# Kernel optimization log

Hardware: AMD Instinct MI355X
Metric: run time of the kernel (lower is better)

Reference implementation:

```python
import jax, jax.numpy as jnp
from jax import lax
import numpy as np

BLOCK_SIZE = 11   # cv2 blockSize (odd)
CONSTANT = 2.0    # cv2 C
MAXVAL = 255.0


def _box_mean(x, k):
    """Local k x k mean with BORDER_REPLICATE, matching cv2 ADAPTIVE_THRESH_MEAN_C.
    x: [N,H,W,1] float32. Separable 1-D box filters for efficiency."""
    pad = k // 2
    xp = jnp.pad(x, ((0, 0), (pad, pad), (pad, pad), (0, 0)), mode='edge')
    kh = jnp.full((k, 1, 1, 1), 1.0 / k, dtype=x.dtype)  # HWIO
    kw = jnp.full((1, k, 1, 1), 1.0 / k, dtype=x.dtype)
    dn = ('NHWC', 'HWIO', 'NHWC')
    y = lax.conv_general_dilated(xp, kh, (1, 1), 'VALID', dimension_numbers=dn)
    y = lax.conv_general_dilated(y, kw, (1, 1), 'VALID', dimension_numbers=dn)
    return y  # [N,H,W,1]


def setup_inputs() -> dict:
    key = jax.random.key(0)
    # grayscale pixel intensities in [0, 255]
    x = jax.random.uniform(key, (128, 512, 512, 1), dtype=jnp.float32) * 255.0
    return {"x": x}


def reference(x):
    # cv2.adaptiveThreshold(..., ADAPTIVE_THRESH_MEAN_C, THRESH_BINARY_INV, blockSize, C):
    #   T(x,y) = mean_{kxk}(src) - C
    #   dst = 0 if src > T else maxValue
    thresh = _box_mean(x, BLOCK_SIZE) - CONSTANT
    out = jnp.where(x > thresh, jnp.float32(0.0), jnp.float32(MAXVAL))
    return out
```

## Files before the change

### kernel.cpp

```cpp
#include <hip/hip_runtime.h>


constexpr int W   = 512;
constexpr int H   = 512;
constexpr int PAD = 5;
constexpr int KS  = 11;
constexpr int TPB = 256;
constexpr int RPB = 32;
constexpr int WP  = W + 2 * PAD;

__global__ __launch_bounds__(TPB)
void AdaptiveThresholding_57904749085171_kernel(const float* __restrict__ x,
                                                float* __restrict__ out)
{
    __shared__ float mv[2][WP];

    const int t  = (int)threadIdx.x;
    const int cA = t;
    const int cB = t + 256;
    const int y0 = (int)blockIdx.x * RPB;
    const size_t ioff = (size_t)blockIdx.y * (size_t)(W * H);
    const float* __restrict__ xi = x + ioff;
    float* __restrict__ oi = out + ioff;
    const float wv = (float)(1.0 / 11.0);

    float r0[KS], r1[KS];

    #pragma unroll
    for (int k = 0; k < KS - 1; ++k) {
        int j = y0 - PAD + k;
        int src = j < 0 ? 0 : (j >= H ? H - 1 : j);
        const float* rp = xi + (size_t)src * W;
        r0[k] = rp[cA];
        r1[k] = rp[cB];
    }
    float p0, p1;
    {
        int j = y0 + PAD;
        int src = j >= H ? H - 1 : j;
        const float* rp = xi + (size_t)src * W;
        p0 = rp[cA];
        p1 = rp[cB];
    }

    for (int y = y0; y < y0 + RPB; ++y) {
        r0[KS - 1] = p0;
        r1[KS - 1] = p1;

        float a0 = 0.0f, a1 = 0.0f;
        #pragma unroll
        for (int d = 0; d < KS; ++d) {
            a0 = fmaf(r0[d], wv, a0);
            a1 = fmaf(r1[d], wv, a1);
        }

        const int pp = (y - y0) & 1;
        mv[pp][PAD + cA] = a0;
        mv[pp][PAD + cB] = a1;
        if (t == 0) {
            #pragma unroll
            for (int i = 0; i < PAD; ++i) mv[pp][i] = a0;
        } else if (t == TPB - 1) {
            #pragma unroll
            for (int i = 0; i < PAD; ++i) mv[pp][W + PAD + i] = a1;
        }

        const float xv0 = r0[PAD];
        const float xv1 = r1[PAD];

        if (y + 1 < y0 + RPB) {
            int j = y + 1 + PAD;
            int src = j >= H ? H - 1 : j;
            const float* rp = xi + (size_t)src * W;
            p0 = rp[cA];
            p1 = rp[cB];
        }

        #pragma unroll
        for (int d = 0; d < KS - 1; ++d) {
            r0[d] = r0[d + 1];
            r1[d] = r1[d + 1];
        }

        __syncthreads();

        float m0 = 0.0f, m1 = 0.0f;
        #pragma unroll
        for (int e = 0; e < KS; ++e) m0 = fmaf(mv[pp][cA + e], wv, m0);
        #pragma unroll
        for (int e = 0; e < KS; ++e) m1 = fmaf(mv[pp][cB + e], wv, m1);

        float* op = oi + (size_t)y * W;
        op[cA] = (xv0 > m0 - 2.0f) ? 0.0f : 255.0f;
        op[cB] = (xv1 > m1 - 2.0f) ? 0.0f : 255.0f;
    }
}

extern "C" void kernel_launch(void* const* d_in, const int* in_sizes, int n_in,
                              void* d_out, int out_size, void* d_ws, size_t ws_size,
                              hipStream_t stream)
{
    const float* x = (const float*)d_in[0];
    float* out = (float*)d_out;
    const int n_imgs = in_sizes[0] / (W * H);

    dim3 grid(H / RPB, n_imgs);
    dim3 block(TPB);
    AdaptiveThresholding_57904749085171_kernel<<<grid, block, 0, stream>>>(x, out);
}
```

Baseline: 55.28 us.

## Process two rows per iteration with interleaved float2 shared buffer and ring registers

Each loop iteration now computes two output rows. The vertical sums for both rows are stored as a float2 pair per column in shared memory, which halves the number of barriers and turns LDS reads into 64-bit accesses. The register window becomes a 12-entry ring buffer indexed at compile time through full unrolling, replacing the per-row shift of registers. Prefetch now loads two rows ahead. The cost is more registers, and the 64-bit LDS accesses may change the bank-conflict pattern.

```diff
diff --git a/kernel.cpp b/kernel.cpp
--- a/kernel.cpp
+++ b/kernel.cpp
@@ -5,15 +5,17 @@
 constexpr int H   = 512;
 constexpr int PAD = 5;
 constexpr int KS  = 11;
+constexpr int RS  = 12;
 constexpr int TPB = 256;
 constexpr int RPB = 32;
+constexpr int PH  = RPB / 2;
 constexpr int WP  = W + 2 * PAD;
 
 __global__ __launch_bounds__(TPB)
 void AdaptiveThresholding_57904749085171_kernel(const float* __restrict__ x,
                                                 float* __restrict__ out)
 {
-    __shared__ float mv[2][WP];
+    __shared__ float mvp[2][WP][2];
 
     const int t  = (int)threadIdx.x;
     const int cA = t;
@@ -24,75 +26,96 @@
     float* __restrict__ oi = out + ioff;
     const float wv = (float)(1.0 / 11.0);
 
-    float r0[KS], r1[KS];
+    float r0[RS], r1[RS];
+    float p0a, p0b, p1a, p1b;
 
     #pragma unroll
-    for (int k = 0; k < KS - 1; ++k) {
-        int j = y0 - PAD + k;
-        int src = j < 0 ? 0 : (j >= H ? H - 1 : j);
+    for (int j = 0; j < 10; ++j) {
+        int v = y0 - PAD + j;
+        int src = v < 0 ? 0 : (v >= H ? H - 1 : v);
         const float* rp = xi + (size_t)src * W;
-        r0[k] = rp[cA];
-        r1[k] = rp[cB];
+        r0[j] = rp[cA];
+        r1[j] = rp[cB];
     }
-    float p0, p1;
     {
-        int j = y0 + PAD;
-        int src = j >= H ? H - 1 : j;
+        int v = y0 + 5;  int src = v >= H ? H - 1 : v;
         const float* rp = xi + (size_t)src * W;
-        p0 = rp[cA];
-        p1 = rp[cB];
+        p0a = rp[cA]; p0b = rp[cB];
+    }
+    {
+        int v = y0 + 6;  int src = v >= H ? H - 1 : v;
+        const float* rp = xi + (size_t)src * W;
+        p1a = rp[cA]; p1b = rp[cB];
     }
 
-    for (int y = y0; y < y0 + RPB; ++y) {
-        r0[KS - 1] = p0;
-        r1[KS - 1] = p1;
+    #pragma unroll
+    for (int k = 0; k < PH; ++k) {
+        const int y = y0 + 2 * k;
 
-        float a0 = 0.0f, a1 = 0.0f;
+        r0[(2 * k + 10) % RS] = p0a;  r1[(2 * k + 10) % RS] = p0b;
+        r0[(2 * k + 11) % RS] = p1a;  r1[(2 * k + 11) % RS] = p1b;
+
+        if (k + 1 < PH) {
+            int v1 = y + 7;  int s1 = v1 >= H ? H - 1 : v1;
+            int v2 = y + 8;  int s2 = v2 >= H ? H - 1 : v2;
+            const float* rp1 = xi + (size_t)s1 * W;
+            const float* rp2 = xi + (size_t)s2 * W;
+            p0a = rp1[cA]; p0b = rp1[cB];
+            p1a = rp2[cA]; p1b = rp2[cB];
+        }
+
+        float aA0 = 0.0f, aB0 = 0.0f, aA1 = 0.0f, aB1 = 0.0f;
         #pragma unroll
         for (int d = 0; d < KS; ++d) {
-            a0 = fmaf(r0[d], wv, a0);
-            a1 = fmaf(r1[d], wv, a1);
+            const int s = (2 * k + d) % RS;
+            aA0 = fmaf(r0[s], wv, aA0);
+            aB0 = fmaf(r1[s], wv, aB0);
+        }
+        #pragma unroll
+        for (int d = 0; d < KS; ++d) {
+            const int s = (2 * k + 1 + d) % RS;
+            aA1 = fmaf(r0[s], wv, aA1);
+            aB1 = fmaf(r1[s], wv, aB1);
         }
 
-        const int pp = (y - y0) & 1;
-        mv[pp][PAD + cA] = a0;
-        mv[pp][PAD + cB] = a1;
+        const int pp = k & 1;
+        *(float2*)&mvp[pp][PAD + cA][0] = make_float2(aA0, aA1);
+        *(float2*)&mvp[pp][PAD + cB][0] = make_float2(aB0, aB1);
         if (t == 0) {
             #pragma unroll
-            for (int i = 0; i < PAD; ++i) mv[pp][i] = a0;
+            for (int i = 0; i < PAD; ++i)
+                *(float2*)&mvp[pp][i][0] = make_float2(aA0, aA1);
         } else if (t == TPB - 1) {
             #pragma unroll
-            for (int i = 0; i < PAD; ++i) mv[pp][W + PAD + i] = a1;
+            for (int i = 0; i < PAD; ++i)
+                *(float2*)&mvp[pp][W + PAD + i][0] = make_float2(aB0, aB1);
         }
 
-        const float xv0 = r0[PAD];
-        const float xv1 = r1[PAD];
-
-        if (y + 1 < y0 + RPB) {
-            int j = y + 1 + PAD;
-            int src = j >= H ? H - 1 : j;
-            const float* rp = xi + (size_t)src * W;
-            p0 = rp[cA];
-            p1 = rp[cB];
-        }
-
-        #pragma unroll
-        for (int d = 0; d < KS - 1; ++d) {
-            r0[d] = r0[d + 1];
-            r1[d] = r1[d + 1];
-        }
+        const float xA0 = r0[(2 * k + 5) % RS], xB0 = r1[(2 * k + 5) % RS];
+        const float xA1 = r0[(2 * k + 6) % RS], xB1 = r1[(2 * k + 6) % RS];
 
         __syncthreads();
 
-        float m0 = 0.0f, m1 = 0.0f;
+        float mA0 = 0.0f, mA1 = 0.0f, mB0 = 0.0f, mB1 = 0.0f;
         #pragma unroll
-        for (int e = 0; e < KS; ++e) m0 = fmaf(mv[pp][cA + e], wv, m0);
+        for (int e = 0; e < KS; ++e) {
+            const float2 v = *(const float2*)&mvp[pp][cA + e][0];
+            mA0 = fmaf(v.x, wv, mA0);
+            mA1 = fmaf(v.y, wv, mA1);
+        }
         #pragma unroll
-        for (int e = 0; e < KS; ++e) m1 = fmaf(mv[pp][cB + e], wv, m1);
+        for (int e = 0; e < KS; ++e) {
+            const float2 v = *(const float2*)&mvp[pp][cB + e][0];
+            mB0 = fmaf(v.x, wv, mB0);
+            mB1 = fmaf(v.y, wv, mB1);
+        }
 
-        float* op = oi + (size_t)y * W;
-        op[cA] = (xv0 > m0 - 2.0f) ? 0.0f : 255.0f;
-        op[cB] = (xv1 > m1 - 2.0f) ? 0.0f : 255.0f;
+        float* opr0 = oi + (size_t)y * W;
+        float* opr1 = oi + (size_t)(y + 1) * W;
+        opr0[cA] = (xA0 > mA0 - 2.0f) ? 0.0f : 255.0f;
+        opr0[cB] = (xB0 > mB0 - 2.0f) ? 0.0f : 255.0f;
+        opr1[cA] = (xA1 > mA1 - 2.0f) ? 0.0f : 255.0f;
+        opr1[cB] = (xB1 > mB1 - 2.0f) ? 0.0f : 255.0f;
     }
 }
 
```

Result: faster. 52.14 us, median of 2 (-5.7%).
